# Kernel optimization log

Measured on AMD Instinct MI355X. Metric: run time of the kernel, lower is better.

Reference implementation:

```python
import jax, jax.numpy as jnp
import numpy as np

DECAY = 0.999
EPS = 1e-05


def setup_inputs() -> dict:
    key = jax.random.key(0)
    k1, k2 = jax.random.split(key)
    B, L, S, D, E = 32, 8, 512, 256, 2048
    x = jax.random.normal(k1, (B, L, S, D), dtype=jnp.float32)
    # stacked per-quantizer codebooks: embed[l] is the [dim, n_embed] buffer of Quantize l
    embed = jax.random.normal(k2, (L, D, E), dtype=jnp.float32)
    cluster_size = jnp.zeros((L, E), dtype=jnp.float32)
    embed_avg = embed.copy()
    return {"x": x, "embed": embed, "cluster_size": cluster_size, "embed_avg": embed_avg}


def reference(x, embed, cluster_size, embed_avg):
    # x: [B, L, S, D]; embed: [L, D, E]; cluster_size: [L, E]; embed_avg: [L, D, E]
    B, L, S, D = x.shape
    E = embed.shape[-1]

    dist = ((x * x).sum(-1, keepdims=True)
            - 2.0 * jnp.einsum('blsd,lde->blse', x, embed)
            + (embed * embed).sum(1)[None, :, None, :])
    ids = jnp.argmin(dist, axis=-1)  # argmax of -dist == argmin of dist; [B, L, S]

    # codebook lookup: embed_t[l, ids[b,l,s]] -> [B, L, S, D]
    embed_t = jnp.swapaxes(embed, 1, 2)  # [L, E, D]
    q = embed_t[jnp.arange(L)[None, :, None], ids]

    # EMA buffer updates (training mode; done on .data in torch, i.e. no grad)
    l_idx = jnp.broadcast_to(jnp.arange(L)[None, :, None], (B, L, S))
    counts = jnp.zeros((L, E), x.dtype).at[l_idx, ids].add(1.0)  # onehot.sum(0) per quantizer
    embed_sum = jnp.zeros((L, E, D), x.dtype).at[l_idx, ids].add(jax.lax.stop_gradient(x))
    embed_sum = jnp.swapaxes(embed_sum, 1, 2)  # [L, D, E] == flatten.T @ onehot
    new_cluster_size = DECAY * cluster_size + (1.0 - DECAY) * counts
    new_embed_avg = DECAY * embed_avg + (1.0 - DECAY) * embed_sum
    n = new_cluster_size.sum(-1, keepdims=True)  # [L, 1]
    cs = (new_cluster_size + EPS) / (n + E * EPS) * n
    new_embed = new_embed_avg / cs[:, None, :]

    # NOTE: the original loop overwrites `diff` each iteration then does `diff += diff`,
    # so the returned diff is 2 * diff_of_last_quantizer / length (faithfully reproduced).
    diff_last = jnp.mean((jax.lax.stop_gradient(q[:, L - 1]) - x[:, L - 1]) ** 2)
    diff = 2.0 * diff_last / L

    # straight-through estimator
    out = x + jax.lax.stop_gradient(q - x)
    return out, diff, ids, new_embed, new_cluster_size, new_embed_avg
```

## Files before the change

kernel.cpp:

```cpp
#include <hip/hip_runtime.h>

#define LL 8
#define BB 32
#define SS 512
#define DD 256
#define EE 2048
#define LED (LL*DD*EE)
#define LE  (LL*EE)
#define NROWS (BB*LL*SS)
#define NSEG 33

typedef __bf16 bf16x8 __attribute__((ext_vector_type(8)));
typedef float  f32x16 __attribute__((ext_vector_type(16)));

__global__ void prep_transpose_kernel(const float* __restrict__ embed,
                                      float* __restrict__ embed_t,
                                      float* __restrict__ norms,
                                      __bf16* __restrict__ frag) {
    __shared__ float tile[32][33];
    const int l  = blockIdx.z;
    const int d0 = blockIdx.y * 32;
    const int e0 = blockIdx.x * 32;
    const int tx = threadIdx.x, ty = threadIdx.y;

    float v = embed[((size_t)l*DD + d0 + ty)*EE + e0 + tx];
    tile[ty][tx] = v;
    __syncthreads();

    embed_t[((size_t)l*EE + e0 + ty)*DD + d0 + tx] = tile[tx][ty];

    const int t    = ty*32 + tx;
    const int ksl  = t >> 9;
    const int pos  = t & 511;
    const int lane = pos >> 3, j = pos & 7;
    const int klocal = (lane >> 5)*8 + j;
    const int e_loc  = lane & 31;
    float val = tile[ksl*16 + klocal][e_loc];
    __bf16 h = (__bf16)val;
    const int m  = blockIdx.x;
    const int ks = (d0 >> 4) + ksl;
    size_t segbase = (((size_t)(l*64 + m))*NSEG + 2*ks)*512 + pos;
    frag[segbase]       = h;
    frag[segbase + 512] = (__bf16)(val - (float)h);

    if (ty == 0) {
        float s = 0.f;
        #pragma unroll
        for (int i = 0; i < 32; ++i) s += tile[i][tx]*tile[i][tx];
        atomicAdd(&norms[l*EE + e0 + tx], s);
    }
}

__global__ void norm_seg_kernel(const float* __restrict__ norms,
                                __bf16* __restrict__ frag) {
    const int bid  = blockIdx.x;
    const int lane = threadIdx.x;
    bf16x8 v;
    #pragma unroll
    for (int j = 0; j < 8; ++j) v[j] = (__bf16)0.0f;
    if (lane < 32) {
        float nv = -0.5f * norms[(bid >> 6)*EE + (bid & 63)*32 + lane];
        __bf16 h = (__bf16)nv;
        v[0] = h;
        v[1] = (__bf16)(nv - (float)h);
    }
    *(bf16x8*)(frag + ((size_t)bid*NSEG + 32)*512 + lane*8) = v;
}

__global__ __launch_bounds__(256, 2)
void argmin_mfma(const float* __restrict__ x,
                 const __bf16* __restrict__ frag,
                 const float* __restrict__ embed_t,
                 int* __restrict__ ids_out,
                 int* __restrict__ counts_i,
                 float* __restrict__ out,
                 float* __restrict__ diff_acc) {
    __shared__ __bf16 slots[2][NSEG*512];

    const int tid  = threadIdx.x;
    const int wave = tid >> 6, lane = tid & 63;
    const int l    = blockIdx.x & 7;
    const int rb   = blockIdx.x >> 3;
    const int idx  = rb*4 + wave;
    const int b    = idx >> 4, st = idx & 15;
    const int rowtile = (b*LL + l)*16 + st;

    bf16x8 bh[17], bl[16];
    {
        const float* xr = x + (size_t)(rowtile*32 + (lane & 31))*DD + (lane >> 5)*8;
        #pragma unroll
        for (int ks = 0; ks < 16; ++ks) {
            float4 v0 = *(const float4*)(xr + ks*16);
            float4 v1 = *(const float4*)(xr + ks*16 + 4);
            float f[8] = {v0.x, v0.y, v0.z, v0.w, v1.x, v1.y, v1.z, v1.w};
            #pragma unroll
            for (int j = 0; j < 8; ++j) {
                __bf16 h = (__bf16)f[j];
                bh[ks][j] = h;
                bl[ks][j] = (__bf16)(f[j] - (float)h);
            }
        }
        #pragma unroll
        for (int j = 0; j < 8; ++j) bh[16][j] = (__bf16)0.0f;
        if (lane < 32) { bh[16][0] = (__bf16)1.0f; bh[16][1] = (__bf16)1.0f; }
    }

    const __bf16* fl = frag + (size_t)l*64*NSEG*512;

    auto stage = [&](int m, int buf) {
        const __bf16* src = fl + (size_t)m*NSEG*512 + lane*8;
        __bf16* dst = &slots[buf][0];
        for (int i = wave; i < NSEG; i += 4) {
            __builtin_amdgcn_global_load_lds(
                (const __attribute__((address_space(1))) void*)(src + i*512),
                (__attribute__((address_space(3))) void*)(dst + i*512), 16, 0, 0);
        }
    };

    float maxv = -1e30f;
    int   maxi = 0;

    auto step = [&](int m, f32x16& Pc, f32x16& Qc, f32x16& Pp, f32x16& Qp) {
        #pragma unroll
        for (int i = 0; i < 16; ++i) { Pc[i] = 0.0f; Qc[i] = 0.0f; }
        if (m < 63) stage(m + 1, (m & 1) ^ 1);
        const __bf16* sA = &slots[m & 1][0];
        const int pbase = (m - 1)*32 + 4*(lane >> 5);

        bf16x8 ah = *(const bf16x8*)(sA + 0*512 + lane*8);
        bf16x8 al = *(const bf16x8*)(sA + 1*512 + lane*8);
        #pragma unroll
        for (int k = 0; k < 16; ++k) {
            bf16x8 nh, nl;
            if (k < 15) {
                nh = *(const bf16x8*)(sA + (2*k + 2)*512 + lane*8);
                nl = *(const bf16x8*)(sA + (2*k + 3)*512 + lane*8);
            } else {
                nh = *(const bf16x8*)(sA + 32*512 + lane*8);
                nl = nh;
            }
            Pc = __builtin_amdgcn_mfma_f32_32x32x16_bf16(ah, bh[k], Pc, 0, 0, 0);
            Qc = __builtin_amdgcn_mfma_f32_32x32x16_bf16(ah, bl[k], Qc, 0, 0, 0);
            Pc = __builtin_amdgcn_mfma_f32_32x32x16_bf16(al, bh[k], Pc, 0, 0, 0);
            {
                float v = Pp[k] + Qp[k];
                int e = pbase + (k & 3) + 8*(k >> 2);
                if (v > maxv) { maxv = v; maxi = e; }
            }
            ah = nh; al = nl;
            if (k < 15) __builtin_amdgcn_sched_group_barrier(0x100, 2, 0);
            else        __builtin_amdgcn_sched_group_barrier(0x100, 1, 0);
            __builtin_amdgcn_sched_group_barrier(0x008, 3, 0);
            __builtin_amdgcn_sched_group_barrier(0x002, 8, 0);
        }
        Pc = __builtin_amdgcn_mfma_f32_32x32x16_bf16(ah, bh[16], Pc, 0, 0, 0);
        __syncthreads();
    };

    f32x16 PA, QA, PB, QB;
    #pragma unroll
    for (int i = 0; i < 16; ++i) { PB[i] = -1e30f; QB[i] = -1e30f; }

    stage(0, 0);
    __syncthreads();

    #pragma unroll 1
    for (int t = 0; t < 32; ++t) {
        step(2*t,     PA, QA, PB, QB);
        step(2*t + 1, PB, QB, PA, QA);
    }
    {
        const int pbase = 63*32 + 4*(lane >> 5);
        #pragma unroll
        for (int k = 0; k < 16; ++k) {
            float v = PB[k] + QB[k];
            int e = pbase + (k & 3) + 8*(k >> 2);
            if (v > maxv) { maxv = v; maxi = e; }
        }
    }

    float ov = __shfl_xor(maxv, 32, 64);
    int   oi = __shfl_xor(maxi, 32, 64);
    if (ov > maxv || (ov == maxv && oi < maxi)) { maxv = ov; maxi = oi; }
    if (lane < 32) {
        ids_out[(size_t)rowtile*32 + lane] = maxi;
        atomicAdd(&counts_i[l*EE + maxi], 1);
    }

    const float4* et4  = (const float4*)embed_t;
    const float4* x4   = (const float4*)x;
    float4*       out4 = (float4*)out;
    float sq = 0.f;
    #pragma unroll 4
    for (int r = 0; r < 32; ++r) {
        int id = __shfl(maxi, r);
        float4 qv = et4[((size_t)l*EE + id)*64 + lane];
        size_t o = ((size_t)rowtile*32 + r)*64 + lane;
        out4[o] = qv;
        if (l == LL - 1) {
            float4 xv = x4[o];
            float dx = qv.x - xv.x, dy = qv.y - xv.y, dz = qv.z - xv.z, dw = qv.w - xv.w;
            sq += dx*dx + dy*dy + dz*dz + dw*dw;
        }
    }
    if (l == LL - 1) {
        #pragma unroll
        for (int off = 32; off; off >>= 1) sq += __shfl_down(sq, off);
        if (lane == 0) atomicAdd(diff_acc, sq);
    }
}

__global__ __launch_bounds__(256)
void scan_kernel(const int* __restrict__ counts_i,
                 const float* __restrict__ cs_in,
                 int* __restrict__ bin_start,
                 int* __restrict__ cursor,
                 float* __restrict__ ncs_out,
                 float* __restrict__ n_out) {
    __shared__ int part[256];
    __shared__ float red[4];
    const int l = blockIdx.x, tid = threadIdx.x;
    const int base = l*EE + tid*8;
    int local[8], tsum = 0;
    float fsum = 0.f;
    #pragma unroll
    for (int j = 0; j < 8; ++j) {
        local[j] = counts_i[base + j];
        tsum += local[j];
        float v = 0.999f*cs_in[base + j] + 0.001f*(float)local[j];
        ncs_out[base + j] = v;
        fsum += v;
    }
    part[tid] = tsum;
    __syncthreads();
    for (int off = 1; off < 256; off <<= 1) {
        int v = (tid >= off) ? part[tid - off] : 0;
        __syncthreads();
        part[tid] += v;
        __syncthreads();
    }
    int run = part[tid] - tsum;
    #pragma unroll
    for (int j = 0; j < 8; ++j) {
        bin_start[base + j] = run;
        cursor[base + j]    = run;
        run += local[j];
    }
    #pragma unroll
    for (int off = 32; off; off >>= 1) fsum += __shfl_down(fsum, off);
    if ((tid & 63) == 0) red[tid >> 6] = fsum;
    __syncthreads();
    if (tid == 0) n_out[l] = red[0] + red[1] + red[2] + red[3];
}

__global__ __launch_bounds__(256)
void scatter_idx_kernel(const int* __restrict__ ids,
                        int* __restrict__ cursor,
                        int* __restrict__ sorted_rows) {
    const int r = blockIdx.x*256 + threadIdx.x;
    const int l = (r >> 9) & 7;
    const int e = ids[r];
    int pos = atomicAdd(&cursor[l*EE + e], 1);
    sorted_rows[l*(NROWS/LL) + pos] = r;
}

__global__ __launch_bounds__(256)
void segsum_kernel(const float* __restrict__ x,
                   const int* __restrict__ sorted_rows,
                   const int* __restrict__ bin_start,
                   const int* __restrict__ counts_i,
                   float* __restrict__ embed_sum) {
    const int bid = blockIdx.x;
    const int l   = bid >> 11;
    const int e   = bid & 2047;
    const int tid = threadIdx.x;
    const int start = bin_start[l*EE + e];
    const int cnt   = counts_i[l*EE + e];
    const int* rows = sorted_rows + l*(NROWS/LL);

    float acc = 0.f;
    int i = 0;
    for (; i + 1 < cnt; i += 2) {
        int r0 = rows[start + i], r1 = rows[start + i + 1];
        acc += x[(size_t)r0*DD + tid] + x[(size_t)r1*DD + tid];
    }
    if (i < cnt) acc += x[(size_t)rows[start + i]*DD + tid];
    embed_sum[((size_t)l*EE + e)*DD + tid] = acc;
}

__global__ void finalize_embed_kernel(const float* __restrict__ embed_avg,
                                      const float* __restrict__ embed_sum,
                                      const float* __restrict__ ncs,
                                      const float* __restrict__ n,
                                      float* __restrict__ nea_out,
                                      float* __restrict__ ne_out) {
    __shared__ float tile[32][33];
    const int l  = blockIdx.z;
    const int d0 = blockIdx.y * 32;
    const int e0 = blockIdx.x * 32;
    const int tx = threadIdx.x, ty = threadIdx.y;

    tile[ty][tx] = embed_sum[((size_t)l*EE + e0 + ty)*DD + d0 + tx];
    __syncthreads();
    const size_t idx = ((size_t)l*DD + d0 + ty)*EE + e0 + tx;
    float nea = 0.999f*embed_avg[idx] + 0.001f*tile[tx][ty];
    nea_out[idx] = nea;
    float nl = n[l];
    float c  = ncs[l*EE + e0 + tx];
    float cs = (c + 1e-5f) / (nl + 0.02048f) * nl;
    ne_out[idx] = nea / cs;
}

__global__ void diff_scale_kernel(const float* __restrict__ diff_acc,
                                  float* __restrict__ diff_out) {
    *diff_out = (*diff_acc / (float)(BB*SS*DD)) * 0.25f;
}

extern "C" void kernel_launch(void* const* d_in, const int* in_sizes, int n_in,
                              void* d_out, int out_size, void* d_ws, size_t ws_size,
                              hipStream_t stream) {
    const float* x            = (const float*)d_in[0];
    const float* embed        = (const float*)d_in[1];
    const float* cluster_size = (const float*)d_in[2];
    const float* embed_avg    = (const float*)d_in[3];

    float* out      = (float*)d_out;
    float* diff_out = out + 33554432;
    int*   ids_out  = (int*)(out + 33554433);
    float* ne_out   = out + 33685505;
    float* ncs_out  = out + 37879809;
    float* nea_out  = out + 37896193;

    float* ws        = (float*)d_ws;
    float* embed_t   = ws;
    float* embed_sum = ws + LED;
    int*   counts_i  = (int*)(ws + 2*(size_t)LED);
    float* norms     = ws + 2*(size_t)LED + LE;
    float* diff_acc  = norms + LE;
    float* n_ws      = diff_acc + 1;
    int*   bin_start = (int*)(n_ws + LL);
    int*   cursor    = bin_start + LE;
    int*   sorted_rows = cursor + LE;
    __bf16* embfrag  = (__bf16*)(sorted_rows + NROWS + 16);

    hipMemsetAsync(counts_i, 0, (size_t)(2*LE + 1) * sizeof(float), stream);

    prep_transpose_kernel<<<dim3(EE/32, DD/32, LL), dim3(32, 32), 0, stream>>>(
        embed, embed_t, norms, embfrag);

    norm_seg_kernel<<<LL*64, 64, 0, stream>>>(norms, embfrag);

    argmin_mfma<<<1024, 256, 0, stream>>>(x, embfrag, embed_t, ids_out,
                                          counts_i, out, diff_acc);

    scan_kernel<<<LL, 256, 0, stream>>>(counts_i, cluster_size, bin_start, cursor,
                                        ncs_out, n_ws);

    scatter_idx_kernel<<<NROWS/256, 256, 0, stream>>>(ids_out, cursor, sorted_rows);

    segsum_kernel<<<LE, 256, 0, stream>>>(x, sorted_rows, bin_start, counts_i, embed_sum);

    finalize_embed_kernel<<<dim3(EE/32, DD/32, LL), dim3(32, 32), 0, stream>>>(
        embed_avg, embed_sum, ncs_out, n_ws, nea_out, ne_out);

    diff_scale_kernel<<<1, 1, 0, stream>>>(diff_acc, diff_out);
}
```

Measured before the change: 945.0 us.

## Load codebook fragments directly from global memory instead of LDS double-buffering

Removes the shared-memory double buffer fed by global_load_lds, along with the per-step __syncthreads and the manual scheduling barriers. Each wave now reads its bf16 codebook fragments straight from global memory (L2/cache) as MFMA operands. This drops the LDS footprint and block-wide syncs, which may allow more waves per CU and removes barrier stalls. The cost is that all four waves fetch the same fragments redundantly, and global-load latency is no longer hidden by explicit prefetching.

```diff
diff --git a/kernel.cpp b/kernel.cpp
--- a/kernel.cpp
+++ b/kernel.cpp
@@ -75,8 +75,6 @@
                  int* __restrict__ counts_i,
                  float* __restrict__ out,
                  float* __restrict__ diff_acc) {
-    __shared__ __bf16 slots[2][NSEG*512];
-
     const int tid  = threadIdx.x;
     const int wave = tid >> 6, lane = tid & 63;
     const int l    = blockIdx.x & 7;
@@ -105,40 +103,20 @@
         if (lane < 32) { bh[16][0] = (__bf16)1.0f; bh[16][1] = (__bf16)1.0f; }
     }
 
-    const __bf16* fl = frag + (size_t)l*64*NSEG*512;
-
-    auto stage = [&](int m, int buf) {
-        const __bf16* src = fl + (size_t)m*NSEG*512 + lane*8;
-        __bf16* dst = &slots[buf][0];
-        for (int i = wave; i < NSEG; i += 4) {
-            __builtin_amdgcn_global_load_lds(
-                (const __attribute__((address_space(1))) void*)(src + i*512),
-                (__attribute__((address_space(3))) void*)(dst + i*512), 16, 0, 0);
-        }
-    };
+    const bf16x8* fseg = (const bf16x8*)(frag + (size_t)l*64*NSEG*512) + lane;
 
     float maxv = -1e30f;
     int   maxi = 0;
 
     auto step = [&](int m, f32x16& Pc, f32x16& Qc, f32x16& Pp, f32x16& Qp) {
+        const bf16x8* sm = fseg + (size_t)m*NSEG*64;
         #pragma unroll
         for (int i = 0; i < 16; ++i) { Pc[i] = 0.0f; Qc[i] = 0.0f; }
-        if (m < 63) stage(m + 1, (m & 1) ^ 1);
-        const __bf16* sA = &slots[m & 1][0];
         const int pbase = (m - 1)*32 + 4*(lane >> 5);
-
-        bf16x8 ah = *(const bf16x8*)(sA + 0*512 + lane*8);
-        bf16x8 al = *(const bf16x8*)(sA + 1*512 + lane*8);
         #pragma unroll
         for (int k = 0; k < 16; ++k) {
-            bf16x8 nh, nl;
-            if (k < 15) {
-                nh = *(const bf16x8*)(sA + (2*k + 2)*512 + lane*8);
-                nl = *(const bf16x8*)(sA + (2*k + 3)*512 + lane*8);
-            } else {
-                nh = *(const bf16x8*)(sA + 32*512 + lane*8);
-                nl = nh;
-            }
+            bf16x8 ah = sm[(2*k    )*64];
+            bf16x8 al = sm[(2*k + 1)*64];
             Pc = __builtin_amdgcn_mfma_f32_32x32x16_bf16(ah, bh[k], Pc, 0, 0, 0);
             Qc = __builtin_amdgcn_mfma_f32_32x32x16_bf16(ah, bl[k], Qc, 0, 0, 0);
             Pc = __builtin_amdgcn_mfma_f32_32x32x16_bf16(al, bh[k], Pc, 0, 0, 0);
@@ -147,22 +125,14 @@
                 int e = pbase + (k & 3) + 8*(k >> 2);
                 if (v > maxv) { maxv = v; maxi = e; }
             }
-            ah = nh; al = nl;
-            if (k < 15) __builtin_amdgcn_sched_group_barrier(0x100, 2, 0);
-            else        __builtin_amdgcn_sched_group_barrier(0x100, 1, 0);
-            __builtin_amdgcn_sched_group_barrier(0x008, 3, 0);
-            __builtin_amdgcn_sched_group_barrier(0x002, 8, 0);
         }
-        Pc = __builtin_amdgcn_mfma_f32_32x32x16_bf16(ah, bh[16], Pc, 0, 0, 0);
-        __syncthreads();
+        bf16x8 an = sm[32*64];
+        Pc = __builtin_amdgcn_mfma_f32_32x32x16_bf16(an, bh[16], Pc, 0, 0, 0);
     };
 
     f32x16 PA, QA, PB, QB;
     #pragma unroll
     for (int i = 0; i < 16; ++i) { PB[i] = -1e30f; QB[i] = -1e30f; }
-
-    stage(0, 0);
-    __syncthreads();
 
     #pragma unroll 1
     for (int t = 0; t < 32; ++t) {
```

After: 1.224 ms. +29.5%, slower.
